# Optimization experiments

Measured on AMD Instinct MI355X. Metric: run time of the kernel, lower is better.

Reference implementation:

```python
import jax, jax.numpy as jnp
import numpy as np

B, T, D = 8, 2048, 256
K, CS = 4, 1024  # num_codebooks, codebook_size


def setup_inputs() -> dict:
    key = jax.random.key(0)
    k_z, k_cb = jax.random.split(key)
    z = jax.random.normal(k_z, (B, T, D), dtype=jnp.float32)
    # original initializes each codebook with jax.random.uniform
    codebooks = jax.random.uniform(k_cb, (K, CS, D), dtype=jnp.float32)
    return {"z": z, "codebooks": codebooks}


def _rvq(z, codebooks):
    def step(residual, cb):
        # GEMM-based squared L2 distance: ||r||^2 - 2 r.c + ||c||^2.
        # ||r||^2 is constant over the codebook axis -> drop it for argmin.
        dist = jnp.sum(cb * cb, axis=-1)[None, None, :] \
            - 2.0 * jnp.einsum('btd,cd->btc', residual, cb)  # [B,T,CS]
        idx = jnp.argmin(dist, axis=-1)          # [B,T]
        q = cb[idx]                              # [B,T,D] gather
        z_q = residual + jax.lax.stop_gradient(q - residual)  # STE per stage
        return residual - z_q, (z_q, idx)

    _, (quants, indices) = jax.lax.scan(step, z, codebooks)
    z_q_final = jnp.sum(quants, axis=0)          # sum over stages
    z_q_final = z + jax.lax.stop_gradient(z_q_final - z)  # outer STE
    all_indices = jnp.moveaxis(indices, 0, -1)   # [B,T,K]
    return z_q_final, all_indices


def reference(z, codebooks):
    return _rvq(z, codebooks)
```

## Files before the change

kernel.cpp:

```cpp
#include <hip/hip_runtime.h>
#include <hip/hip_bf16.h>

#define DD 256
#define KK 4
#define CSZ 1024
#define NROWS 16384
#define TM 64
#define NTHR 512
#define TAU 0.5f
#define MAXC 192

typedef __attribute__((ext_vector_type(8))) short bf16x8;
typedef __attribute__((ext_vector_type(4))) float f32x4;

__device__ __forceinline__ short f2bf(float f) {
    __hip_bfloat16 h = __float2bfloat16(f);
    return (short)__builtin_bit_cast(unsigned short, h);
}
__device__ __forceinline__ unsigned long long enc_d(double d) {
    unsigned long long u = __double_as_longlong(d);
    return (u & 0x8000000000000000ull) ? ~u : (u | 0x8000000000000000ull);
}

__global__ __launch_bounds__(256) void cb_pack(const float* __restrict__ cb,
                                               short* __restrict__ packed) {
    int idx  = blockIdx.x * 256 + threadIdx.x;
    int lane = idx & 63;
    int kk   = (idx >> 6) & 7;
    int tg   = idx >> 9;
    int k    = tg >> 6;
    int ctg  = tg & 63;
    int c    = ctg * 16 + (lane & 15);
    int d0   = kk * 32 + (lane >> 4) * 8;
    const float* src = cb + ((size_t)(k * CSZ + c)) * DD + d0;
    short* dst = packed + (size_t)idx * 8;
#pragma unroll
    for (int j = 0; j < 8; ++j) dst[j] = f2bf(src[j]);
}

__global__ __launch_bounds__(256) void cnorm_kernel(const float* __restrict__ cb,
                                                    double* __restrict__ cn_d,
                                                    float* __restrict__ cn_f) {
    int wv = threadIdx.x >> 6, l = threadIdx.x & 63;
    int e = blockIdx.x * 4 + wv;
    float4 v = *(const float4*)(cb + (size_t)e * DD + l * 4);
    double s = (double)v.x * (double)v.x + (double)v.y * (double)v.y
             + (double)v.z * (double)v.z + (double)v.w * (double)v.w;
#pragma unroll
    for (int off = 32; off > 0; off >>= 1) s += __shfl_xor(s, off, 64);
    if (l == 0) { cn_d[e] = s; cn_f[e] = (float)s; }
}

#define LOADB(Bv, CNv, ct_) {                                         \
    const short* bp_ = pkk + (size_t)((seg >> 4) + (ct_)) * 4096 + l * 8; \
    _Pragma("unroll")                                                 \
    for (int kk = 0; kk < 8; ++kk)                                    \
        Bv[kk] = *(const bf16x8*)(bp_ + kk * 512);                    \
    CNv = cnfk[seg + (ct_) * 16 + l15]; }

#define KUPD(rt_, dval) {                                             \
    float dc_ = fmaxf((dval), 0.f);                                   \
    unsigned kx_ = (__builtin_bit_cast(unsigned, dc_) & 0xFFFFFC00u)  \
                   | (unsigned)cE_;                                   \
    unsigned mx_ = (b0[rt_][reg] > kx_) ? b0[rt_][reg] : kx_;         \
    b0[rt_][reg] = (b0[rt_][reg] < kx_) ? b0[rt_][reg] : kx_;         \
    b1[rt_][reg] = (b1[rt_][reg] < mx_) ? b1[rt_][reg] : mx_; }

#define TILE2(Bv, CNv, ct_) {                                         \
    f32x4 ac0 = {0.f,0.f,0.f,0.f}, ac1 = {0.f,0.f,0.f,0.f};           \
    _Pragma("unroll")                                                 \
    for (int kk = 0; kk < 8; ++kk) {                                  \
        ac0 = __builtin_amdgcn_mfma_f32_16x16x32_bf16(A[0][kk], Bv[kk], ac0, 0,0,0); \
        ac1 = __builtin_amdgcn_mfma_f32_16x16x32_bf16(A[1][kk], Bv[kk], ac1, 0,0,0); \
    }                                                                 \
    const int cE_ = seg + (ct_) * 16 + l15;                           \
    _Pragma("unroll")                                                 \
    for (int reg = 0; reg < 4; ++reg) {                               \
        KUPD(0, fmaf(-2.f, ac0[reg], CNv));                           \
        KUPD(1, fmaf(-2.f, ac1[reg], CNv));                           \
    } }

__global__ __launch_bounds__(NTHR, 2) void rvq_kernel(const float* __restrict__ z,
                                                  const float* __restrict__ cb,
                                                  const short* __restrict__ packed,
                                                  const double* __restrict__ cn_d,
                                                  const float* __restrict__ cn_f,
                                                  int* __restrict__ idx_ws,
                                                  float* __restrict__ out) {
    __shared__ double res_d[TM][DD + 1];
    __shared__ unsigned wrowmin[8][TM];
    __shared__ int cand[MAXC];
    __shared__ unsigned long long rowkey[2][TM];
    __shared__ int ncand;

    const int tid = threadIdx.x;
    const int l   = tid & 63;
    const int wv  = tid >> 6;
    const int rtp = wv & 1;
    const int l15 = l & 15;
    const int q   = l >> 4;
    const int q8  = q * 8;
    const int row0 = blockIdx.x * TM;
    const int seg  = (wv >> 1) * 256;
    const int hrow = tid >> 8;
    const int hd   = tid & 255;

#pragma unroll 4
    for (int it = 0; it < TM / 2; ++it) {
        int r = it * 2 + hrow;
        res_d[r][hd] = (double)z[(size_t)(row0 + r) * DD + hd];
    }
    if (tid < TM) { rowkey[0][tid] = ~0ull; rowkey[1][tid] = ~0ull; }
    if (tid == 0) ncand = 0;
    __syncthreads();

    for (int k = 0; k < KK; ++k) {
        const int kb = k & 1;
        bf16x8 A[2][8];
#pragma unroll
        for (int rtl = 0; rtl < 2; ++rtl)
#pragma unroll
            for (int kk = 0; kk < 8; ++kk) {
                const double* rp = &res_d[rtp * 32 + rtl * 16 + l15][kk * 32 + q8];
#pragma unroll
                for (int j = 0; j < 8; ++j)
                    A[rtl][kk][j] = f2bf((float)rp[j]);
            }

        const short* __restrict__ pkk  = packed + (size_t)k * CSZ * DD;
        const float* __restrict__ cnfk = cn_f + k * CSZ;
        unsigned b0[2][4], b1[2][4];
#pragma unroll
        for (int rtl = 0; rtl < 2; ++rtl)
#pragma unroll
            for (int reg = 0; reg < 4; ++reg) { b0[rtl][reg] = ~0u; b1[rtl][reg] = ~0u; }

        bf16x8 Bp[8], Bq[8];
        float cnP, cnQ;
        LOADB(Bp, cnP, 0);
        for (int ct2 = 0; ct2 < 8; ++ct2) {
            LOADB(Bq, cnQ, 2 * ct2 + 1);
            TILE2(Bp, cnP, 2 * ct2);
            if (ct2 < 7) LOADB(Bp, cnP, 2 * ct2 + 2);
            TILE2(Bq, cnQ, 2 * ct2 + 1);
        }

#pragma unroll
        for (int rtl = 0; rtl < 2; ++rtl)
#pragma unroll
            for (int reg = 0; reg < 4; ++reg) {
                unsigned m = b0[rtl][reg];
                m = min(m, (unsigned)__shfl_xor((int)m, 1, 64));
                m = min(m, (unsigned)__shfl_xor((int)m, 2, 64));
                m = min(m, (unsigned)__shfl_xor((int)m, 4, 64));
                m = min(m, (unsigned)__shfl_xor((int)m, 8, 64));
                if (l15 == 0) wrowmin[wv][rtp * 32 + rtl * 16 + q * 4 + reg] = m;
            }
        __syncthreads();

#pragma unroll
        for (int rtl = 0; rtl < 2; ++rtl)
#pragma unroll
            for (int reg = 0; reg < 4; ++reg) {
                const int row = rtp * 32 + rtl * 16 + q * 4 + reg;
                unsigned rk = min(min(wrowmin[rtp][row], wrowmin[rtp + 2][row]),
                                  min(wrowmin[rtp + 4][row], wrowmin[rtp + 6][row]));
                float thrf = __builtin_bit_cast(float, rk | 0x3FFu) + TAU;
                unsigned tkey = (__builtin_bit_cast(unsigned, thrf) & 0xFFFFFC00u) | 0x3FFu;
                if (b0[rtl][reg] <= tkey) {
                    int sl = atomicAdd(&ncand, 1);
                    if (sl < MAXC) cand[sl] = row | ((int)(b0[rtl][reg] & 0x3FFu) << 16);
                }
                if (b1[rtl][reg] <= tkey) {
                    int sl = atomicAdd(&ncand, 1);
                    if (sl < MAXC) cand[sl] = row | ((int)(b1[rtl][reg] & 0x3FFu) << 16);
                }
            }
        __syncthreads();

        const int nc = (ncand < MAXC) ? ncand : MAXC;
        const float* __restrict__ cbk   = cb + (size_t)k * CSZ * DD;
        const double* __restrict__ cndk = cn_d + k * CSZ;
        const int g = tid >> 4;
        for (int i = g; i < nc; i += 32) {
            int rc  = cand[i];
            int row = rc & 0xFFFF;
            int c   = rc >> 16;
            const float* crow = cbk + (size_t)c * DD;
            double p = 0.0;
#pragma unroll
            for (int ii = 0; ii < 16; ++ii)
                p += res_d[row][ii * 16 + l15] * (double)crow[ii * 16 + l15];
            p += __shfl_xor(p, 1, 64);
            p += __shfl_xor(p, 2, 64);
            p += __shfl_xor(p, 4, 64);
            p += __shfl_xor(p, 8, 64);
            if (l15 == 0) {
                double dist = cndk[c] - 2.0 * p;
                unsigned long long key =
                    (enc_d(dist) & 0xFFFFFFFFFFFFFC00ull) | (unsigned long long)c;
                atomicMin(&rowkey[kb][row], key);
            }
        }
        __syncthreads();

        if (tid < TM)
            idx_ws[(size_t)(row0 + tid) * KK + k] = (int)(rowkey[kb][tid] & 1023ull);
#pragma unroll 4
        for (int it = 0; it < TM / 2; ++it) {
            int r = it * 2 + hrow;
            int c = (int)(rowkey[kb][r] & 1023ull);
            double qv = (double)cbk[(size_t)c * DD + hd];
            double rd = res_d[r][hd];
            double s  = qv - rd;
            double zq = rd + s;
            res_d[r][hd] = rd - zq;
        }
        if (tid < TM) rowkey[kb ^ 1][tid] = ~0ull;
        if (tid == 0) ncand = 0;
        __syncthreads();
    }

#pragma unroll 4
    for (int it = 0; it < TM / 2; ++it) {
        int r = it * 2 + hrow;
        size_t o = (size_t)(row0 + r) * DD + hd;
        out[o] = (float)((double)z[o] - res_d[r][hd]);
    }
}

__global__ __launch_bounds__(256) void idx_write(const int* __restrict__ idx_ws,
                                                 float* __restrict__ out) {
    int i = blockIdx.x * 256 + threadIdx.x;
    out[(long)NROWS * DD + i] = (float)idx_ws[i];
}

extern "C" void kernel_launch(void* const* d_in, const int* in_sizes, int n_in,
                              void* d_out, int out_size, void* d_ws, size_t ws_size,
                              hipStream_t stream) {
    (void)in_sizes; (void)n_in; (void)out_size; (void)ws_size;
    const float* z  = (const float*)d_in[0];
    const float* cb = (const float*)d_in[1];

    char* ws = (char*)d_ws;
    short*  packed = (short*)ws;
    double* cn_d  = (double*)(ws + (size_t)2 * 1024 * 1024);
    float*  cn_f  = (float*)(ws + (size_t)2 * 1024 * 1024 + 32 * 1024);
    int*    idxs  = (int*)(ws + (size_t)2 * 1024 * 1024 + 48 * 1024);
    float* out = (float*)d_out;

    cb_pack<<<(KK * 64 * 8 * 64) / 256, 256, 0, stream>>>(cb, packed);
    cnorm_kernel<<<(KK * CSZ) / 4, 256, 0, stream>>>(cb, cn_d, cn_f);
    rvq_kernel<<<NROWS / TM, NTHR, 0, stream>>>(z, cb, packed, cn_d, cn_f, idxs, out);
    idx_write<<<(NROWS * KK) / 256, 256, 0, stream>>>(idxs, out);
}
```

Baseline: 104.2 us.

## Halve rows per block and split codebook across all eight waves

Measured after the change: 186.2 us. +78.7%, slower.

```diff
diff --git a/kernel.cpp b/kernel.cpp
--- a/kernel.cpp
+++ b/kernel.cpp
@@ -5,7 +5,7 @@
 #define KK 4
 #define CSZ 1024
 #define NROWS 16384
-#define TM 64
+#define TM 32
 #define NTHR 512
 #define TAU 0.5f
 #define MAXC 192
@@ -51,12 +51,12 @@
     if (l == 0) { cn_d[e] = s; cn_f[e] = (float)s; }
 }
 
-#define LOADB(Bv, CNv, ct_) {                                         \
-    const short* bp_ = pkk + (size_t)((seg >> 4) + (ct_)) * 4096 + l * 8; \
+#define LOADB(Bv, CNv, t_) {                                          \
+    const short* bp_ = pkk + (size_t)(t_) * 4096 + l * 8;             \
     _Pragma("unroll")                                                 \
     for (int kk = 0; kk < 8; ++kk)                                    \
         Bv[kk] = *(const bf16x8*)(bp_ + kk * 512);                    \
-    CNv = cnfk[seg + (ct_) * 16 + l15]; }
+    CNv = cnfk[(t_) * 16 + l15]; }
 
 #define KUPD(rt_, dval) {                                             \
     float dc_ = fmaxf((dval), 0.f);                                   \
@@ -66,14 +66,14 @@
     b0[rt_][reg] = (b0[rt_][reg] < kx_) ? b0[rt_][reg] : kx_;         \
     b1[rt_][reg] = (b1[rt_][reg] < mx_) ? b1[rt_][reg] : mx_; }
 
-#define TILE2(Bv, CNv, ct_) {                                         \
+#define TILE2(Bv, CNv, t_) {                                          \
     f32x4 ac0 = {0.f,0.f,0.f,0.f}, ac1 = {0.f,0.f,0.f,0.f};           \
     _Pragma("unroll")                                                 \
     for (int kk = 0; kk < 8; ++kk) {                                  \
         ac0 = __builtin_amdgcn_mfma_f32_16x16x32_bf16(A[0][kk], Bv[kk], ac0, 0,0,0); \
         ac1 = __builtin_amdgcn_mfma_f32_16x16x32_bf16(A[1][kk], Bv[kk], ac1, 0,0,0); \
     }                                                                 \
-    const int cE_ = seg + (ct_) * 16 + l15;                           \
+    const int cE_ = (t_) * 16 + l15;                                  \
     _Pragma("unroll")                                                 \
     for (int reg = 0; reg < 4; ++reg) {                               \
         KUPD(0, fmaf(-2.f, ac0[reg], CNv));                           \
@@ -96,12 +96,10 @@
     const int tid = threadIdx.x;
     const int l   = tid & 63;
     const int wv  = tid >> 6;
-    const int rtp = wv & 1;
     const int l15 = l & 15;
     const int q   = l >> 4;
     const int q8  = q * 8;
     const int row0 = blockIdx.x * TM;
-    const int seg  = (wv >> 1) * 256;
     const int hrow = tid >> 8;
     const int hd   = tid & 255;
 
@@ -121,7 +119,7 @@
         for (int rtl = 0; rtl < 2; ++rtl)
 #pragma unroll
             for (int kk = 0; kk < 8; ++kk) {
-                const double* rp = &res_d[rtp * 32 + rtl * 16 + l15][kk * 32 + q8];
+                const double* rp = &res_d[rtl * 16 + l15][kk * 32 + q8];
 #pragma unroll
                 for (int j = 0; j < 8; ++j)
                     A[rtl][kk][j] = f2bf((float)rp[j]);
@@ -135,14 +133,18 @@
 #pragma unroll
             for (int reg = 0; reg < 4; ++reg) { b0[rtl][reg] = ~0u; b1[rtl][reg] = ~0u; }
 
-        bf16x8 Bp[8], Bq[8];
-        float cnP, cnQ;
-        LOADB(Bp, cnP, 0);
-        for (int ct2 = 0; ct2 < 8; ++ct2) {
-            LOADB(Bq, cnQ, 2 * ct2 + 1);
-            TILE2(Bp, cnP, 2 * ct2);
-            if (ct2 < 7) LOADB(Bp, cnP, 2 * ct2 + 2);
-            TILE2(Bq, cnQ, 2 * ct2 + 1);
+        {
+            const int t0 = wv * 8;
+            bf16x8 Bp[8], Bq[8];
+            float cnP, cnQ;
+            LOADB(Bp, cnP, t0);
+#pragma unroll
+            for (int ct2 = 0; ct2 < 4; ++ct2) {
+                LOADB(Bq, cnQ, t0 + 2 * ct2 + 1);
+                TILE2(Bp, cnP, t0 + 2 * ct2);
+                if (ct2 < 3) LOADB(Bp, cnP, t0 + 2 * ct2 + 2);
+                TILE2(Bq, cnQ, t0 + 2 * ct2 + 1);
+            }
         }
 
 #pragma unroll
@@ -154,7 +156,7 @@
                 m = min(m, (unsigned)__shfl_xor((int)m, 2, 64));
                 m = min(m, (unsigned)__shfl_xor((int)m, 4, 64));
                 m = min(m, (unsigned)__shfl_xor((int)m, 8, 64));
-                if (l15 == 0) wrowmin[wv][rtp * 32 + rtl * 16 + q * 4 + reg] = m;
+                if (l15 == 0) wrowmin[wv][rtl * 16 + q * 4 + reg] = m;
             }
         __syncthreads();
 
@@ -162,9 +164,11 @@
         for (int rtl = 0; rtl < 2; ++rtl)
 #pragma unroll
             for (int reg = 0; reg < 4; ++reg) {
-                const int row = rtp * 32 + rtl * 16 + q * 4 + reg;
-                unsigned rk = min(min(wrowmin[rtp][row], wrowmin[rtp + 2][row]),
-                                  min(wrowmin[rtp + 4][row], wrowmin[rtp + 6][row]));
+                const int row = rtl * 16 + q * 4 + reg;
+                unsigned rk = min(min(min(wrowmin[0][row], wrowmin[1][row]),
+                                      min(wrowmin[2][row], wrowmin[3][row])),
+                                  min(min(wrowmin[4][row], wrowmin[5][row]),
+                                      min(wrowmin[6][row], wrowmin[7][row])));
                 float thrf = __builtin_bit_cast(float, rk | 0x3FFu) + TAU;
                 unsigned tkey = (__builtin_bit_cast(unsigned, thrf) & 0xFFFFFC00u) | 0x3FFu;
                 if (b0[rtl][reg] <= tkey) {
```
